# Kernel tuning notes

Measured on AMD Instinct MI355X. Metric: run time of the kernel, lower is better.

Reference implementation:

```python
import jax, jax.numpy as jnp
import numpy as np
import math

B, N, K, S = 4, 128, 250, 250   # batch, channels(d_model), chunk len, num chunks
M = 64 // 2                      # d_state complex modes (conjugate-pair S4D param.)


def setup_inputs() -> dict:
    key = jax.random.key(0)
    ks = jax.random.split(key, 24)
    d = {"x": jax.random.normal(ks[0], (B, N, K, S), jnp.float32)}
    i = 1
    for p in ("intra", "inter"):
        # S4D (diagonal SSM) parameters
        d[p + "_log_dt"] = (jax.random.uniform(ks[i], (N,), jnp.float32)
                            * (math.log(0.1) - math.log(0.001)) + math.log(0.001))
        d[p + "_logA_re"] = jnp.full((N, M), math.log(0.5), jnp.float32)
        d[p + "_A_im"] = jnp.tile(math.pi * jnp.arange(M, dtype=jnp.float32), (N, 1))
        d[p + "_C_re"] = jax.random.normal(ks[i + 1], (N, M), jnp.float32) * (0.5 ** 0.5)
        d[p + "_C_im"] = jax.random.normal(ks[i + 2], (N, M), jnp.float32) * (0.5 ** 0.5)
        d[p + "_D"] = jax.random.normal(ks[i + 3], (N,), jnp.float32)
        # S4 output position-wise linear (H -> 2H) + GLU
        d[p + "_ow"] = jax.random.normal(ks[i + 4], (2 * N, N), jnp.float32) / math.sqrt(N)
        d[p + "_ob"] = jnp.zeros((2 * N,), jnp.float32)
        # block linear
        d[p + "_lw"] = jax.random.normal(ks[i + 5], (N, N), jnp.float32) / math.sqrt(N)
        d[p + "_lb"] = jnp.zeros((N,), jnp.float32)
        # GroupNorm(1, N)
        d[p + "_gg"] = jnp.ones((N,), jnp.float32)
        d[p + "_gb"] = jnp.zeros((N,), jnp.float32)
        i += 6
    return d


def _s4(u, log_dt, logA_re, A_im, C_re, C_im, D, ow, ob):
    # u: [b, H, L] (transposed layout). S4D kernel + FFT conv + GELU + GLU out.
    L = u.shape[-1]
    dt = jnp.exp(log_dt)                              # [H]
    A = -jnp.exp(logA_re) + 1j * A_im                 # [H, M]
    dtA = dt[:, None] * A                             # [H, M]
    C = (C_re + 1j * C_im) * (jnp.exp(dtA) - 1.0) / A # ZOH-discretized C
    vand = jnp.exp(dtA[:, :, None] * jnp.arange(L, dtype=jnp.float32))  # [H, M, L]
    kern = 2.0 * jnp.einsum('hm,hml->hl', C, vand).real                 # [H, L]
    n = 2 * L
    y = jnp.fft.irfft(jnp.fft.rfft(u, n) * jnp.fft.rfft(kern, n), n)[..., :L]
    y = y + D[:, None] * u
    y = jax.nn.gelu(y)
    y = jnp.einsum('oh,bhl->bol', ow, y) + ob[None, :, None]            # [b, 2H, L]
    y1, y2 = jnp.split(y, 2, axis=1)
    return y1 * jax.nn.sigmoid(y2)                                      # GLU -> [b, H, L]


def _group_norm(x, g, b, eps=1e-8):
    mu = jnp.mean(x, axis=(1, 2, 3), keepdims=True)
    var = jnp.var(x, axis=(1, 2, 3), keepdims=True)
    return (x - mu) / jnp.sqrt(var + eps) * g[None, :, None, None] + b[None, :, None, None]


def reference(x,
              intra_log_dt, intra_logA_re, intra_A_im, intra_C_re, intra_C_im,
              intra_D, intra_ow, intra_ob, intra_lw, intra_lb, intra_gg, intra_gb,
              inter_log_dt, inter_logA_re, inter_A_im, inter_C_re, inter_C_im,
              inter_D, inter_ow, inter_ob, inter_lw, inter_lb, inter_gg, inter_gb):
    Bx, Nx, Kx, Sx = x.shape
    # intra (within-chunk) path: sequence length = K
    intra = jnp.transpose(x, (0, 3, 1, 2)).reshape(Bx * Sx, Nx, Kx)
    intra = _s4(intra, intra_log_dt, intra_logA_re, intra_A_im,
                intra_C_re, intra_C_im, intra_D, intra_ow, intra_ob)
    # faithful to torch: .view(B*S*K, -1) on contiguous [B*S, N, K]
    intra = (intra.reshape(Bx * Sx * Kx, -1) @ intra_lw.T + intra_lb).reshape(Bx * Sx, Nx, Kx)
    intra = jnp.transpose(intra.reshape(Bx, Sx, Nx, Kx), (0, 2, 3, 1))  # [B,N,K,S]
    intra = _group_norm(intra, intra_gg, intra_gb) + x
    # inter (across-chunk) path: sequence length = S
    inter = jnp.transpose(intra, (0, 2, 1, 3)).reshape(Bx * Kx, Nx, Sx)
    inter = _s4(inter, inter_log_dt, inter_logA_re, inter_A_im,
                inter_C_re, inter_C_im, inter_D, inter_ow, inter_ob)
    inter = (inter.reshape(Bx * Kx * Sx, -1) @ inter_lw.T + inter_lb).reshape(Bx * Kx, Nx, Sx)
    inter = jnp.transpose(inter.reshape(Bx, Kx, Nx, Sx), (0, 2, 1, 3))  # [B,N,K,S]
    inter = _group_norm(inter, inter_gg, inter_gb)
    return inter + intra
```

## Files before the change

kernel.cpp:

```cpp
#include <hip/hip_runtime.h>
#include <math.h>

#define NTOT 32000000

typedef __attribute__((ext_vector_type(8))) short bf8_t;
typedef __attribute__((ext_vector_type(4))) float f4_t;

__device__ __forceinline__ float fast_tanh(float t) {
    return 1.0f - 2.0f / (1.0f + __expf(2.0f * t));
}
__device__ __forceinline__ float gelu_f(float v) {
    return 0.5f * v * (1.0f + fast_tanh(0.7978845608028654f * (v + 0.044715f * v * v * v)));
}
__device__ __forceinline__ float sigmoid_f(float v) {
    return 1.0f / (1.0f + __expf(-v));
}
__device__ __forceinline__ unsigned short f2bf(float f) {
    unsigned u = __float_as_uint(f);
    u = (u + 0x7FFFu + ((u >> 16) & 1u)) >> 16;
    return (unsigned short)u;
}
__device__ __forceinline__ float bf2f(unsigned short u) {
    return __uint_as_float(((unsigned)u) << 16);
}
__device__ __forceinline__ unsigned swz(unsigned a) {
    return a ^ (((a >> 9) & 7u) << 4);
}

__global__ void wc_kernel(const float* __restrict__ log_dt, const float* __restrict__ logA_re,
                          const float* __restrict__ A_im, const float* __restrict__ C_re,
                          const float* __restrict__ C_im, float* __restrict__ wC) {
    int t = blockIdx.x * 256 + threadIdx.x;
    if (t >= 128 * 32) return;
    int h = t >> 5, m = t & 31;
    float dt  = expf(log_dt[h]);
    float are = -expf(logA_re[t]);
    float aim = A_im[t];
    float er  = expf(dt * are);
    float wr  = er * cosf(dt * aim);
    float wi  = er * sinf(dt * aim);
    float e1r = wr - 1.0f, e1i = wi;
    float inv = 1.0f / (are * are + aim * aim);
    float qr  = (e1r * are + e1i * aim) * inv;
    float qi  = (e1i * are - e1r * aim) * inv;
    float cre = C_re[t], cim = C_im[t];
    wC[h * 128 + m]      = dt * are;
    wC[h * 128 + 32 + m] = dt * aim;
    wC[h * 128 + 64 + m] = 2.0f * (cre * qr - cim * qi);
    wC[h * 128 + 96 + m] = 2.0f * (cre * qi + cim * qr);
}

__global__ void kern_kernel(const float* __restrict__ wC, const float* __restrict__ Dv,
                            float* __restrict__ kern) {
    int h = blockIdx.x, l = threadIdx.x;
    const float* wc = wC + (h << 7);
    float acc = 0.0f;
    if (l < 250) {
        float fl = (float)l;
#pragma unroll 1
        for (int m = 0; m < 32; ++m) {
            float er  = expf(wc[m] * fl);
            float ang = wc[32 + m] * fl;
            float sv, cv;
            sincosf(ang, &sv, &cv);
            acc += er * (wc[64 + m] * cv - wc[96 + m] * sv);
        }
        if (l == 0) acc += Dv[h];
    }
    kern[(h << 8) + l] = acc;
}

__global__ void frag_kernel(const float* __restrict__ kern, unsigned short* __restrict__ fragH,
                            unsigned short* __restrict__ fragL) {
    int h = blockIdx.x, d16 = blockIdx.y, lane = threadIdx.x;
    int lid = lane & 15, q = lane >> 4;
    const float* kh = kern + (h << 8);
    bf8_t vh, vl;
#pragma unroll
    for (int j = 0; j < 8; ++j) {
        int idx = d16 * 16 + lid - 8 * q - j;
        float v = (idx >= 0) ? kh[idx] : 0.0f;
        unsigned short hb = f2bf(v);
        vh[j] = (short)hb;
        vl[j] = (short)f2bf(v - bf2f(hb));
    }
    long off = ((long)((h << 4) + d16) * 64 + lane) * 8;
    *(bf8_t*)(fragH + off) = vh;
    *(bf8_t*)(fragL + off) = vl;
}

__global__ void cvtw_kernel(const float* __restrict__ ow, const float* __restrict__ lw,
                            unsigned short* __restrict__ owbf, unsigned short* __restrict__ lwbf) {
    int t = blockIdx.x * 256 + threadIdx.x;
    if (t < 32768) owbf[t] = f2bf(ow[t]);
    else if (t < 49152) lwbf[t - 32768] = f2bf(lw[t - 32768]);
}

__global__ __launch_bounds__(256, 3)
void conv_kernel(const float* __restrict__ in, unsigned short* __restrict__ Y,
                 const unsigned short* __restrict__ fragH, const unsigned short* __restrict__ fragL,
                 int inter) {
    __shared__ unsigned short Bhi[64 * 256];
    __shared__ unsigned short Blo[64 * 40];
    const int tid = threadIdx.x;
    const int lane = tid & 63, wave = tid >> 6;
    const int lid = lane & 15, quad = lane >> 4;
    const int a = wave >> 1, p = wave & 1;
    const int s0 = blockIdx.x * 64;
    const int h = blockIdx.y, b = blockIdx.z;
    const float* src = in + (long)(b * 128 + h) * 62500;
    char* BhiB = (char*)Bhi;
    char* BloB = (char*)Blo;

    f4_t acc[4][4];
#pragma unroll
    for (int rt = 0; rt < 4; ++rt)
#pragma unroll
        for (int ct = 0; ct < 4; ++ct) acc[rt][ct] = (f4_t)0.0f;

    float2 pf[4];
    auto loadc = [&](int c) {
        if (!inter) {
#pragma unroll
            for (int it = 0; it < 4; ++it) {
                int i = tid + it * 256;
                int kk = i >> 5;
                int sp = (i & 31) << 1;
                int k = (c << 5) + kk;
                bool v = (k < 250) && (s0 + sp < 250);
                pf[it] = v ? *(const float2*)(src + (long)k * 250 + s0 + sp)
                           : make_float2(0.0f, 0.0f);
            }
        } else {
#pragma unroll
            for (int it = 0; it < 4; ++it) {
                int i = tid + it * 256;
                int sq = i >> 4;
                int tt = (i & 15) << 1;
                int t = (c << 5) + tt;
                bool v = (s0 + sq < 250) && (t < 250);
                pf[it] = v ? *(const float2*)(src + (long)(s0 + sq) * 250 + t)
                           : make_float2(0.0f, 0.0f);
            }
        }
    };
    auto storec = [&](int c) {
        if (!inter) {
#pragma unroll
            for (int it = 0; it < 4; ++it) {
                int i = tid + it * 256;
                int kk = i >> 5;
                int sp = (i & 31) << 1;
                int k = (c << 5) + kk;
                unsigned short hx = f2bf(pf[it].x);
                unsigned short hy = f2bf(pf[it].y);
                unsigned b0 = (unsigned)(sp * 512 + k * 2) ^ ((unsigned)(sp & 7) << 4);
                unsigned b1 = (unsigned)((sp + 1) * 512 + k * 2) ^ ((unsigned)((sp + 1) & 7) << 4);
                *(unsigned short*)(BhiB + b0) = hx;
                *(unsigned short*)(BhiB + b1) = hy;
                Blo[sp * 40 + kk] = f2bf(pf[it].x - bf2f(hx));
                Blo[(sp + 1) * 40 + kk] = f2bf(pf[it].y - bf2f(hy));
            }
        } else {
#pragma unroll
            for (int it = 0; it < 4; ++it) {
                int i = tid + it * 256;
                int sq = i >> 4;
                int tt = (i & 15) << 1;
                unsigned short hx = f2bf(pf[it].x);
                unsigned short hy = f2bf(pf[it].y);
                unsigned hpack = (unsigned)hx | ((unsigned)hy << 16);
                unsigned b0 = (unsigned)(sq * 512 + ((c << 5) + tt) * 2) ^ ((unsigned)(sq & 7) << 4);
                *(unsigned*)(BhiB + b0) = hpack;
                unsigned short lx = f2bf(pf[it].x - bf2f(hx));
                unsigned short ly = f2bf(pf[it].y - bf2f(hy));
                *(unsigned*)(BloB + sq * 80 + tt * 2) = (unsigned)lx | ((unsigned)ly << 16);
            }
        }
    };

    loadc(0);
#pragma unroll 1
    for (int c = 0; c < 8; ++c) {
        __syncthreads();
        storec(c);
        __syncthreads();
        if (c < 7) loadc(c + 1);
        bf8_t bh[4], bl[4];
#pragma unroll
        for (int ct = 0; ct < 4; ++ct) {
            int row = ct * 16 + lid;
            unsigned byteB = (unsigned)(row * 512 + c * 64 + quad * 16) ^ ((unsigned)(row & 7) << 4);
            bh[ct] = *(const bf8_t*)(BhiB + byteB);
            bl[ct] = *(const bf8_t*)(BloB + row * 80 + quad * 16);
        }
#pragma unroll
        for (int rt = 0; rt < 4; ++rt) {
            int n = 2 * rt + a - c;
            if (n >= 0) {
                long fo = ((long)((h << 4) + 2 * n + p) * 64 + lane) * 8;
                bf8_t fh = *(const bf8_t*)(fragH + fo);
                bf8_t fl = *(const bf8_t*)(fragL + fo);
#pragma unroll
                for (int ct = 0; ct < 4; ++ct) {
                    acc[rt][ct] = __builtin_amdgcn_mfma_f32_16x16x32_bf16(fh, bh[ct], acc[rt][ct], 0, 0, 0);
                    acc[rt][ct] = __builtin_amdgcn_mfma_f32_16x16x32_bf16(fh, bl[ct], acc[rt][ct], 0, 0, 0);
                    acc[rt][ct] = __builtin_amdgcn_mfma_f32_16x16x32_bf16(fl, bh[ct], acc[rt][ct], 0, 0, 0);
                }
            }
        }
    }
    __syncthreads();
#pragma unroll
    for (int rt = 0; rt < 4; ++rt) {
        const int l0 = rt * 64 + wave * 16 + quad * 4;
#pragma unroll
        for (int ct = 0; ct < 4; ++ct) {
            const int sq = ct * 16 + lid;
            unsigned lo = (unsigned)f2bf(gelu_f(acc[rt][ct][0])) |
                          ((unsigned)f2bf(gelu_f(acc[rt][ct][1])) << 16);
            unsigned hi = (unsigned)f2bf(gelu_f(acc[rt][ct][2])) |
                          ((unsigned)f2bf(gelu_f(acc[rt][ct][3])) << 16);
            unsigned byteO = (unsigned)(sq * 512 + l0 * 2) ^ ((unsigned)(sq & 7) << 4);
            *(uint2*)(BhiB + byteO) = make_uint2(lo, hi);
        }
    }
    __syncthreads();
    unsigned int* Yg = (unsigned int*)Y + ((long)(b * 250 + s0) * 128 + h) * 125;
#pragma unroll 1
    for (int i = tid; i < 8192; i += 256) {
        int sq = i >> 7, e = i & 127;
        if (e < 125 && s0 + sq < 250) {
            unsigned v = *(unsigned*)(BhiB + ((unsigned)(sq * 512 + e * 4) ^ ((unsigned)(sq & 7) << 4)));
            Yg[(long)sq * 16000 + e] = v;
        }
    }
}

__global__ __launch_bounds__(256, 2)
void mlp_kernel(const unsigned short* __restrict__ Ybf, const unsigned short* __restrict__ owbf,
                const float* __restrict__ ob, const unsigned short* __restrict__ lwbf,
                const float* __restrict__ lb, float* __restrict__ V, double* __restrict__ part) {
    __shared__ unsigned short ZL[32768];
    __shared__ unsigned short Yt[32 * 136];
    const int tid = threadIdx.x;
    const int lane = tid & 63, wave = tid >> 6;
    const int lid = lane & 15, quad = lane >> 4;
    const int seq = blockIdx.x;
    const unsigned short* Ys = Ybf + (long)seq * 32000;

    const int tb0 = 2 * wave;
    int tmap[4] = {tb0, tb0 + 1, tb0 + 8, tb0 + 9};
    bf8_t wf[4][4];
#pragma unroll
    for (int c = 0; c < 4; ++c)
#pragma unroll
        for (int t = 0; t < 4; ++t)
            wf[c][t] = *(const bf8_t*)(owbf + (tmap[t] * 16 + lid) * 128 + c * 32 + quad * 8);
    float ob1[2][4], ob2[2][4];
#pragma unroll
    for (int pp = 0; pp < 2; ++pp)
#pragma unroll
        for (int reg = 0; reg < 4; ++reg) {
            int o = tmap[pp] * 16 + quad * 4 + reg;
            ob1[pp][reg] = ob[o];
            ob2[pp][reg] = ob[128 + o];
        }

    unsigned int pf[8];
    auto loadc = [&](int l0) {
#pragma unroll
        for (int it = 0; it < 8; ++it) {
            int i = tid + it * 256;
            int hh = i >> 4;
            int l = l0 + (i & 15) * 2;
            pf[it] = (l < 250) ? *(const unsigned int*)(Ys + hh * 250 + l) : 0u;
        }
    };
    auto storec = [&]() {
#pragma unroll
        for (int it = 0; it < 8; ++it) {
            int i = tid + it * 256;
            int hh = i >> 4;
            int l2 = (i & 15) * 2;
            Yt[l2 * 136 + hh] = (unsigned short)(pf[it] & 0xFFFF);
            Yt[(l2 + 1) * 136 + hh] = (unsigned short)(pf[it] >> 16);
        }
    };

    loadc(0);
#pragma unroll 1
    for (int ch = 0; ch < 8; ++ch) {
        __syncthreads();
        storec();
        __syncthreads();
        if (ch < 7) loadc((ch + 1) * 32);
        f4_t acc[4][2];
#pragma unroll
        for (int t = 0; t < 4; ++t)
#pragma unroll
            for (int jj = 0; jj < 2; ++jj) acc[t][jj] = (f4_t)0.0f;
#pragma unroll
        for (int c = 0; c < 4; ++c) {
            bf8_t bfr[2];
#pragma unroll
            for (int jj = 0; jj < 2; ++jj)
                bfr[jj] = *(const bf8_t*)(Yt + (jj * 16 + lid) * 136 + c * 32 + quad * 8);
#pragma unroll
            for (int t = 0; t < 4; ++t)
#pragma unroll
                for (int jj = 0; jj < 2; ++jj)
                    acc[t][jj] = __builtin_amdgcn_mfma_f32_16x16x32_bf16(wf[c][t], bfr[jj], acc[t][jj], 0, 0, 0);
        }
        const int lbase = ch * 32;
#pragma unroll
        for (int pp = 0; pp < 2; ++pp) {
#pragma unroll
            for (int reg = 0; reg < 4; ++reg) {
                int o = tmap[pp] * 16 + quad * 4 + reg;
#pragma unroll
                for (int jj = 0; jj < 2; ++jj) {
                    int l = lbase + jj * 16 + lid;
                    if (l < 250) {
                        float z1 = acc[pp][jj][reg] + ob1[pp][reg];
                        float z2 = acc[pp + 2][jj][reg] + ob2[pp][reg];
                        unsigned aB = swz((unsigned)(o * 250 + l) * 2u);
                        *(unsigned short*)((char*)ZL + aB) = f2bf(z1 * sigmoid_f(z2));
                    }
                }
            }
        }
    }
    __syncthreads();

    f4_t acc2[4][8];
#pragma unroll
    for (int mt = 0; mt < 4; ++mt)
#pragma unroll
        for (int nt = 0; nt < 8; ++nt) acc2[mt][nt] = (f4_t)0.0f;
    const int j0 = wave * 64;
#pragma unroll
    for (int c = 0; c < 4; ++c) {
        bf8_t af[4];
#pragma unroll
        for (int mt = 0; mt < 4; ++mt) {
            unsigned aB = swz((unsigned)((j0 + mt * 16 + lid) * 128 + c * 32 + quad * 8) * 2u);
            af[mt] = *(const bf8_t*)((char*)ZL + aB);
        }
#pragma unroll
        for (int nt = 0; nt < 8; ++nt) {
            bf8_t bfr = *(const bf8_t*)(lwbf + (nt * 16 + lid) * 128 + c * 32 + quad * 8);
#pragma unroll
            for (int mt = 0; mt < 4; ++mt)
                acc2[mt][nt] = __builtin_amdgcn_mfma_f32_16x16x32_bf16(af[mt], bfr, acc2[mt][nt], 0, 0, 0);
        }
    }
    double s = 0.0, q = 0.0;
    float* Vs = V + (long)seq * 32000;
#pragma unroll
    for (int nt = 0; nt < 8; ++nt) {
        int o = nt * 16 + lid;
        float bb = lb[o];
#pragma unroll
        for (int mt = 0; mt < 4; ++mt)
#pragma unroll
            for (int reg = 0; reg < 4; ++reg) {
                int j = j0 + mt * 16 + quad * 4 + reg;
                if (j < 250) {
                    float v = acc2[mt][nt][reg] + bb;
                    Vs[j * 128 + o] = v;
                    s += (double)v;
                    q += (double)v * (double)v;
                }
            }
    }
    __syncthreads();
    double* red = (double*)Yt;
    red[tid] = s;
    red[256 + tid] = q;
    __syncthreads();
    for (int st = 128; st > 0; st >>= 1) {
        if (tid < st) {
            red[tid] += red[tid + st];
            red[256 + tid] += red[256 + tid + st];
        }
        __syncthreads();
    }
    if (tid == 0) {
        part[seq * 2] = red[0];
        part[seq * 2 + 1] = red[256];
    }
}

__global__ void stats_final_kernel(const double* __restrict__ part, float* __restrict__ stats) {
    __shared__ double ssum[256], ssq[256];
    const int b = blockIdx.x;
    double s = 0.0, q = 0.0;
    if (threadIdx.x < 250) {
        s = part[(b * 250 + threadIdx.x) * 2];
        q = part[(b * 250 + threadIdx.x) * 2 + 1];
    }
    ssum[threadIdx.x] = s; ssq[threadIdx.x] = q;
    __syncthreads();
    for (int st = 128; st > 0; st >>= 1) {
        if (threadIdx.x < st) {
            ssum[threadIdx.x] += ssum[threadIdx.x + st];
            ssq[threadIdx.x]  += ssq[threadIdx.x + st];
        }
        __syncthreads();
    }
    if (threadIdx.x == 0) {
        double mu = ssum[0] / 8000000.0;
        double var = ssq[0] / 8000000.0 - mu * mu;
        stats[b * 2] = (float)mu;
        stats[b * 2 + 1] = (float)(1.0 / sqrt(var + 1e-8));
    }
}

__global__ void intra_fin_kernel(const float* __restrict__ f, const float* __restrict__ x,
                                 const float* __restrict__ stats, const float* __restrict__ gg,
                                 const float* __restrict__ gb, float* __restrict__ out) {
    __shared__ float tile[32][33];
    int kt = blockIdx.x, st = blockIdx.y;
    int bn = blockIdx.z; int b = bn >> 7, n = bn & 127;
    int tx = threadIdx.x & 31, ty = threadIdx.x >> 5;
    const float mu = stats[b * 2], rs = stats[b * 2 + 1];
    const float ga = gg[n] * rs, bb = gb[n];
    const float* fb = f + (long)(b * 250) * 32000 + n * 250;
#pragma unroll
    for (int j = 0; j < 4; ++j) {
        int k = kt * 32 + tx;
        int s = st * 32 + ty + j * 8;
        if (k < 250 && s < 250) tile[ty + j * 8][tx] = fb[(long)s * 32000 + k];
    }
    __syncthreads();
#pragma unroll
    for (int j = 0; j < 4; ++j) {
        int s = st * 32 + tx;
        int k = kt * 32 + ty + j * 8;
        if (k < 250 && s < 250) {
            long idx = ((long)(b * 128 + n) * 250 + k) * 250 + s;
            out[idx] = (tile[tx][ty + j * 8] - mu) * ga + bb + x[idx];
        }
    }
}

__global__ void final_kernel(const float* __restrict__ f2, const float* __restrict__ stats,
                             const float* __restrict__ gg, const float* __restrict__ gb,
                             float* __restrict__ out) {
    long g = (long)blockIdx.x * 256 + threadIdx.x;
    if (g >= NTOT) return;
    int s = (int)(g % 250); long r = g / 250;
    int k = (int)(r % 250); long bn = r / 250;
    int n = (int)(bn % 128); int b = (int)(bn / 128);
    float mu = stats[b * 2], rs = stats[b * 2 + 1];
    float v = f2[((long)(b * 250 + k) * 128 + n) * 250 + s];
    out[g] = (v - mu) * rs * gg[n] + gb[n] + out[g];
}

extern "C" void kernel_launch(void* const* d_in, const int* in_sizes, int n_in,
                              void* d_out, int out_size, void* d_ws, size_t ws_size,
                              hipStream_t stream) {
    (void)in_sizes; (void)n_in; (void)out_size; (void)ws_size;
    const float* x = (const float*)d_in[0];
    float* out = (float*)d_out;
    char* base = (char*)d_ws;
    float* V            = (float*)base;
    unsigned short* Ybf = (unsigned short*)(base + 128000000L);
    float* wC           = (float*)(base + 256000000L);
    unsigned short* owbf= (unsigned short*)(base + 256065536L);
    unsigned short* lwbf= (unsigned short*)(base + 256131072L);
    double* part        = (double*)(base + 256163840L);
    float* stats        = (float*)(base + 256180224L);
    float* kern         = (float*)(base + 118000000L);
    unsigned short* fragH = (unsigned short*)(base + 120000000L);
    unsigned short* fragL = (unsigned short*)(base + 123000000L);

    const float* i_logdt = (const float*)d_in[1];
    const float* i_logA  = (const float*)d_in[2];
    const float* i_Aim   = (const float*)d_in[3];
    const float* i_Cre   = (const float*)d_in[4];
    const float* i_Cim   = (const float*)d_in[5];
    const float* i_D     = (const float*)d_in[6];
    const float* i_ow    = (const float*)d_in[7];
    const float* i_ob    = (const float*)d_in[8];
    const float* i_lw    = (const float*)d_in[9];
    const float* i_lb    = (const float*)d_in[10];
    const float* i_gg    = (const float*)d_in[11];
    const float* i_gb    = (const float*)d_in[12];
    const float* e_logdt = (const float*)d_in[13];
    const float* e_logA  = (const float*)d_in[14];
    const float* e_Aim   = (const float*)d_in[15];
    const float* e_Cre   = (const float*)d_in[16];
    const float* e_Cim   = (const float*)d_in[17];
    const float* e_D     = (const float*)d_in[18];
    const float* e_ow    = (const float*)d_in[19];
    const float* e_ob    = (const float*)d_in[20];
    const float* e_lw    = (const float*)d_in[21];
    const float* e_lb    = (const float*)d_in[22];
    const float* e_gg    = (const float*)d_in[23];
    const float* e_gb    = (const float*)d_in[24];

    wc_kernel<<<16, 256, 0, stream>>>(i_logdt, i_logA, i_Aim, i_Cre, i_Cim, wC);
    kern_kernel<<<128, 256, 0, stream>>>(wC, i_D, kern);
    frag_kernel<<<dim3(128, 16), 64, 0, stream>>>(kern, fragH, fragL);
    cvtw_kernel<<<192, 256, 0, stream>>>(i_ow, i_lw, owbf, lwbf);
    conv_kernel<<<dim3(4, 128, 4), 256, 0, stream>>>(x, Ybf, fragH, fragL, 0);
    mlp_kernel<<<1000, 256, 0, stream>>>(Ybf, owbf, i_ob, lwbf, i_lb, V, part);
    stats_final_kernel<<<4, 256, 0, stream>>>(part, stats);
    intra_fin_kernel<<<dim3(8, 8, 512), 256, 0, stream>>>(V, x, stats, i_gg, i_gb, out);

    wc_kernel<<<16, 256, 0, stream>>>(e_logdt, e_logA, e_Aim, e_Cre, e_Cim, wC);
    kern_kernel<<<128, 256, 0, stream>>>(wC, e_D, kern);
    frag_kernel<<<dim3(128, 16), 64, 0, stream>>>(kern, fragH, fragL);
    cvtw_kernel<<<192, 256, 0, stream>>>(e_ow, e_lw, owbf, lwbf);
    conv_kernel<<<dim3(4, 128, 4), 256, 0, stream>>>(out, Ybf, fragH, fragL, 1);
    mlp_kernel<<<1000, 256, 0, stream>>>(Ybf, owbf, e_ob, lwbf, e_lb, V, part);
    stats_final_kernel<<<4, 256, 0, stream>>>(part, stats);
    final_kernel<<<NTOT / 256, 256, 0, stream>>>(V, stats, e_gg, e_gb, out);
}
```

Measured before the change: 841.1 us.

## Split MLP kernel across two blocks per sequence and repad LDS swizzles

The MLP kernel is split into two blocks per sequence, each handling half of the GLU hidden channels, which halves its LDS footprint so more blocks can be resident (launch bounds raised to 3). Partial statistics move from double to float and the stats reducer now sums 500 partials. The conv kernel's LDS layouts switch from padding to an XOR swizzle, with packed 8-byte stores of four consecutive k values, and its launch bound is raised to 4 blocks. The aim is higher occupancy and fewer LDS bank conflicts, at the cost of float accumulation in the partial sums and possible register spilling under the tighter bounds.

After: 1.085 ms. +29.0%, slower.

```diff
diff --git a/kernel.cpp b/kernel.cpp
--- a/kernel.cpp
+++ b/kernel.cpp
@@ -25,6 +25,9 @@
 }
 __device__ __forceinline__ unsigned swz(unsigned a) {
     return a ^ (((a >> 9) & 7u) << 4);
+}
+__device__ __forceinline__ unsigned fxor(int row) {
+    return ((unsigned)(row & 1) << 6) ^ ((unsigned)((row >> 1) & 7) << 4);
 }
 
 __global__ void wc_kernel(const float* __restrict__ log_dt, const float* __restrict__ logA_re,
@@ -96,12 +99,12 @@
     else if (t < 49152) lwbf[t - 32768] = f2bf(lw[t - 32768]);
 }
 
-__global__ __launch_bounds__(256, 3)
+__global__ __launch_bounds__(256, 4)
 void conv_kernel(const float* __restrict__ in, unsigned short* __restrict__ Y,
                  const unsigned short* __restrict__ fragH, const unsigned short* __restrict__ fragL,
                  int inter) {
     __shared__ unsigned short Bhi[64 * 256];
-    __shared__ unsigned short Blo[64 * 40];
+    __shared__ unsigned short Blo[64 * 64];
     const int tid = threadIdx.x;
     const int lane = tid & 63, wave = tid >> 6;
     const int lid = lane & 15, quad = lane >> 4;
@@ -111,6 +114,8 @@
     const float* src = in + (long)(b * 128 + h) * 62500;
     char* BhiB = (char*)Bhi;
     char* BloB = (char*)Blo;
+    const int q8 = tid >> 5;
+    const int spL = (tid & 31) << 1;
 
     f4_t acc[4][4];
 #pragma unroll
@@ -123,12 +128,9 @@
         if (!inter) {
 #pragma unroll
             for (int it = 0; it < 4; ++it) {
-                int i = tid + it * 256;
-                int kk = i >> 5;
-                int sp = (i & 31) << 1;
-                int k = (c << 5) + kk;
-                bool v = (k < 250) && (s0 + sp < 250);
-                pf[it] = v ? *(const float2*)(src + (long)k * 250 + s0 + sp)
+                int k = (c << 5) + q8 * 4 + it;
+                bool v = (k < 250) && (s0 + spL < 250);
+                pf[it] = v ? *(const float2*)(src + (long)k * 250 + s0 + spL)
                            : make_float2(0.0f, 0.0f);
             }
         } else {
@@ -146,21 +148,30 @@
     };
     auto storec = [&](int c) {
         if (!inter) {
+            unsigned wx0 = 0, wx1 = 0, wy0 = 0, wy1 = 0;
+            unsigned lx0 = 0, lx1 = 0, ly0 = 0, ly1 = 0;
 #pragma unroll
             for (int it = 0; it < 4; ++it) {
-                int i = tid + it * 256;
-                int kk = i >> 5;
-                int sp = (i & 31) << 1;
-                int k = (c << 5) + kk;
-                unsigned short hx = f2bf(pf[it].x);
-                unsigned short hy = f2bf(pf[it].y);
-                unsigned b0 = (unsigned)(sp * 512 + k * 2) ^ ((unsigned)(sp & 7) << 4);
-                unsigned b1 = (unsigned)((sp + 1) * 512 + k * 2) ^ ((unsigned)((sp + 1) & 7) << 4);
-                *(unsigned short*)(BhiB + b0) = hx;
-                *(unsigned short*)(BhiB + b1) = hy;
-                Blo[sp * 40 + kk] = f2bf(pf[it].x - bf2f(hx));
-                Blo[(sp + 1) * 40 + kk] = f2bf(pf[it].y - bf2f(hy));
-            }
+                unsigned short hx = f2bf(pf[it].x), hy = f2bf(pf[it].y);
+                unsigned short lx = f2bf(pf[it].x - bf2f(hx));
+                unsigned short ly = f2bf(pf[it].y - bf2f(hy));
+                if (it < 2) {
+                    wx0 |= (unsigned)hx << (16 * it); wy0 |= (unsigned)hy << (16 * it);
+                    lx0 |= (unsigned)lx << (16 * it); ly0 |= (unsigned)ly << (16 * it);
+                } else {
+                    wx1 |= (unsigned)hx << (16 * (it - 2)); wy1 |= (unsigned)hy << (16 * (it - 2));
+                    lx1 |= (unsigned)lx << (16 * (it - 2)); ly1 |= (unsigned)ly << (16 * (it - 2));
+                }
+            }
+            unsigned colB = (unsigned)((c << 6) + (q8 << 3));
+            unsigned a0 = ((unsigned)(spL * 512) + colB) ^ fxor(spL);
+            unsigned a1 = ((unsigned)((spL + 1) * 512) + colB) ^ fxor(spL + 1);
+            *(uint2*)(BhiB + a0) = make_uint2(wx0, wx1);
+            *(uint2*)(BhiB + a1) = make_uint2(wy0, wy1);
+            unsigned c0 = ((unsigned)(spL * 128) + (unsigned)(q8 << 3)) ^ fxor(spL);
+            unsigned c1 = ((unsigned)((spL + 1) * 128) + (unsigned)(q8 << 3)) ^ fxor(spL + 1);
+            *(uint2*)(BloB + c0) = make_uint2(lx0, lx1);
+            *(uint2*)(BloB + c1) = make_uint2(ly0, ly1);
         } else {
 #pragma unroll
             for (int it = 0; it < 4; ++it) {
@@ -169,12 +180,12 @@
                 int tt = (i & 15) << 1;
                 unsigned short hx = f2bf(pf[it].x);
                 unsigned short hy = f2bf(pf[it].y);
-                unsigned hpack = (unsigned)hx | ((unsigned)hy << 16);
-                unsigned b0 = (unsigned)(sq * 512 + ((c << 5) + tt) * 2) ^ ((unsigned)(sq & 7) << 4);
-                *(unsigned*)(BhiB + b0) = hpack;
+                unsigned b0 = ((unsigned)(sq * 512 + ((c << 5) + tt) * 2)) ^ fxor(sq);
+                *(unsigned*)(BhiB + b0) = (unsigned)hx | ((unsigned)hy << 16);
                 unsigned short lx = f2bf(pf[it].x - bf2f(hx));
                 unsigned short ly = f2bf(pf[it].y - bf2f(hy));
-                *(unsigned*)(BloB + sq * 80 + tt * 2) = (unsigned)lx | ((unsigned)ly << 16);
+                unsigned b1 = ((unsigned)(sq * 128 + tt * 2)) ^ fxor(sq);
+                *(unsigned*)(BloB + b1) = (unsigned)lx | ((unsigned)ly << 16);
             }
         }
     };
@@ -190,9 +201,8 @@
 #pragma unroll
         for (int ct = 0; ct < 4; ++ct) {
             int row = ct * 16 + lid;
-            unsigned byteB = (unsigned)(row * 512 + c * 64 + quad * 16) ^ ((unsigned)(row & 7) << 4);
-            bh[ct] = *(const bf8_t*)(BhiB + byteB);
-            bl[ct] = *(const bf8_t*)(BloB + row * 80 + quad * 16);
+            bh[ct] = *(const bf8_t*)(BhiB + (((unsigned)(row * 512 + c * 64 + quad * 16)) ^ fxor(row)));
+            bl[ct] = *(const bf8_t*)(BloB + (((unsigned)(row * 128 + quad * 16)) ^ fxor(row)));
         }
 #pragma unroll
         for (int rt = 0; rt < 4; ++rt) {
@@ -221,7 +231,7 @@
                           ((unsigned)f2bf(gelu_f(acc[rt][ct][1])) << 16);
             unsigned hi = (unsigned)f2bf(gelu_f(acc[rt][ct][2])) |
                           ((unsigned)f2bf(gelu_f(acc[rt][ct][3])) << 16);
-            unsigned byteO = (unsigned)(sq * 512 + l0 * 2) ^ ((unsigned)(sq & 7) << 4);
+            unsigned byteO = ((unsigned)(sq * 512 + l0 * 2)) ^ fxor(sq);
             *(uint2*)(BhiB + byteO) = make_uint2(lo, hi);
         }
     }
@@ -231,41 +241,41 @@
     for (int i = tid; i < 8192; i += 256) {
         int sq = i >> 7, e = i & 127;
         if (e < 125 && s0 + sq < 250) {
-            unsigned v = *(unsigned*)(BhiB + ((unsigned)(sq * 512 + e * 4) ^ ((unsigned)(sq & 7) << 4)));
+            unsigned v = *(unsigned*)(BhiB + (((unsigned)(sq * 512 + e * 4)) ^ fxor(sq)));
             Yg[(long)sq * 16000 + e] = v;
         }
     }
 }
 
-__global__ __launch_bounds__(256, 2)
+__global__ __launch_bounds__(256, 3)
 void mlp_kernel(const unsigned short* __restrict__ Ybf, const unsigned short* __restrict__ owbf,
                 const float* __restrict__ ob, const unsigned short* __restrict__ lwbf,
-                const float* __restrict__ lb, float* __restrict__ V, double* __restrict__ part) {
-    __shared__ unsigned short ZL[32768];
-    __shared__ unsigned short Yt[32 * 136];
+                const float* __restrict__ lb, float* __restrict__ V, float* __restrict__ part) {
+    __shared__ unsigned short ZL[16000];
+    __shared__ unsigned short Yt[32 * 128];
     const int tid = threadIdx.x;
     const int lane = tid & 63, wave = tid >> 6;
     const int lid = lane & 15, quad = lane >> 4;
-    const int seq = blockIdx.x;
+    const int seq = blockIdx.x, hf = blockIdx.y;
     const unsigned short* Ys = Ybf + (long)seq * 32000;
-
-    const int tb0 = 2 * wave;
-    int tmap[4] = {tb0, tb0 + 1, tb0 + 8, tb0 + 9};
-    bf8_t wf[4][4];
-#pragma unroll
-    for (int c = 0; c < 4; ++c)
-#pragma unroll
-        for (int t = 0; t < 4; ++t)
-            wf[c][t] = *(const bf8_t*)(owbf + (tmap[t] * 16 + lid) * 128 + c * 32 + quad * 8);
-    float ob1[2][4], ob2[2][4];
-#pragma unroll
-    for (int pp = 0; pp < 2; ++pp)
-#pragma unroll
-        for (int reg = 0; reg < 4; ++reg) {
-            int o = tmap[pp] * 16 + quad * 4 + reg;
-            ob1[pp][reg] = ob[o];
-            ob2[pp][reg] = ob[128 + o];
-        }
+    char* YtB = (char*)Yt;
+    char* ZLB = (char*)ZL;
+
+    const int tA = 4 * hf + wave;
+    const int tB = 8 + 4 * hf + wave;
+    bf8_t wf[4][2];
+#pragma unroll
+    for (int c = 0; c < 4; ++c) {
+        wf[c][0] = *(const bf8_t*)(owbf + (tA * 16 + lid) * 128 + c * 32 + quad * 8);
+        wf[c][1] = *(const bf8_t*)(owbf + (tB * 16 + lid) * 128 + c * 32 + quad * 8);
+    }
+    float ob1[4], ob2[4];
+#pragma unroll
+    for (int reg = 0; reg < 4; ++reg) {
+        int hp = wave * 16 + quad * 4 + reg;
+        ob1[reg] = ob[64 * hf + hp];
+        ob2[reg] = ob[128 + 64 * hf + hp];
+    }
 
     unsigned int pf[8];
     auto loadc = [&](int l0) {
@@ -283,8 +293,10 @@
             int i = tid + it * 256;
             int hh = i >> 4;
             int l2 = (i & 15) * 2;
-            Yt[l2 * 136 + hh] = (unsigned short)(pf[it] & 0xFFFF);
-            Yt[(l2 + 1) * 136 + hh] = (unsigned short)(pf[it] >> 16);
+            unsigned a0 = ((unsigned)(l2 * 256 + hh * 2)) ^ fxor(l2);
+            unsigned a1 = ((unsigned)((l2 + 1) * 256 + hh * 2)) ^ fxor(l2 + 1);
+            *(unsigned short*)(YtB + a0) = (unsigned short)(pf[it] & 0xFFFF);
+            *(unsigned short*)(YtB + a1) = (unsigned short)(pf[it] >> 16);
         }
     };
 
@@ -295,87 +307,87 @@
         storec();
         __syncthreads();
         if (ch < 7) loadc((ch + 1) * 32);
-        f4_t acc[4][2];
-#pragma unroll
-        for (int t = 0; t < 4; ++t)
-#pragma unroll
-            for (int jj = 0; jj < 2; ++jj) acc[t][jj] = (f4_t)0.0f;
+        f4_t acc[2][2];
+#pragma unroll
+        for (int pp = 0; pp < 2; ++pp)
+#pragma unroll
+            for (int jj = 0; jj < 2; ++jj) acc[pp][jj] = (f4_t)0.0f;
 #pragma unroll
         for (int c = 0; c < 4; ++c) {
             bf8_t bfr[2];
 #pragma unroll
-            for (int jj = 0; jj < 2; ++jj)
-                bfr[jj] = *(const bf8_t*)(Yt + (jj * 16 + lid) * 136 + c * 32 + quad * 8);
-#pragma unroll
-            for (int t = 0; t < 4; ++t)
+            for (int jj = 0; jj < 2; ++jj) {
+                int row = jj * 16 + lid;
+                bfr[jj] = *(const bf8_t*)(YtB + (((unsigned)(row * 256 + c * 64 + quad * 16)) ^ fxor(row)));
+            }
+#pragma unroll
+            for (int pp = 0; pp < 2; ++pp)
 #pragma unroll
                 for (int jj = 0; jj < 2; ++jj)
-                    acc[t][jj] = __builtin_amdgcn_mfma_f32_16x16x32_bf16(wf[c][t], bfr[jj], acc[t][jj], 0, 0, 0);
+                    acc[pp][jj] = __builtin_amdgcn_mfma_f32_16x16x32_bf16(wf[c][pp], bfr[jj], acc[pp][jj], 0, 0, 0);
         }
         const int lbase = ch * 32;
 #pragma unroll
-        for (int pp = 0; pp < 2; ++pp) {
-#pragma unroll
-            for (int reg = 0; reg < 4; ++reg) {
-                int o = tmap[pp] * 16 + quad * 4 + reg;
-#pragma unroll
-                for (int jj = 0; jj < 2; ++jj) {
-                    int l = lbase + jj * 16 + lid;
-                    if (l < 250) {
-                        float z1 = acc[pp][jj][reg] + ob1[pp][reg];
-                        float z2 = acc[pp + 2][jj][reg] + ob2[pp][reg];
-                        unsigned aB = swz((unsigned)(o * 250 + l) * 2u);
-                        *(unsigned short*)((char*)ZL + aB) = f2bf(z1 * sigmoid_f(z2));
-                    }
+        for (int reg = 0; reg < 4; ++reg) {
+            int hp = wave * 16 + quad * 4 + reg;
+#pragma unroll
+            for (int jj = 0; jj < 2; ++jj) {
+                int l = lbase + jj * 16 + lid;
+                if (l < 250) {
+                    float z1 = acc[0][jj][reg] + ob1[reg];
+                    float z2 = acc[1][jj][reg] + ob2[reg];
+                    unsigned aB = swz((unsigned)(hp * 250 + l) * 2u);
+                    *(unsigned short*)(ZLB + aB) = f2bf(z1 * sigmoid_f(z2));
                 }
             }
         }
     }
     __syncthreads();
 
-    f4_t acc2[4][8];
-#pragma unroll
-    for (int mt = 0; mt < 4; ++mt)
+    f4_t acc2[2][8];
+#pragma unroll
+    for (int mt = 0; mt < 2; ++mt)
 #pragma unroll
         for (int nt = 0; nt < 8; ++nt) acc2[mt][nt] = (f4_t)0.0f;
-    const int j0 = wave * 64;
+    const int jl0 = wave * 32;
 #pragma unroll
     for (int c = 0; c < 4; ++c) {
-        bf8_t af[4];
-#pragma unroll
-        for (int mt = 0; mt < 4; ++mt) {
-            unsigned aB = swz((unsigned)((j0 + mt * 16 + lid) * 128 + c * 32 + quad * 8) * 2u);
-            af[mt] = *(const bf8_t*)((char*)ZL + aB);
+        bf8_t af[2];
+#pragma unroll
+        for (int mt = 0; mt < 2; ++mt) {
+            int jl = jl0 + mt * 16 + lid;
+            if (jl > 124) jl = 124;
+            af[mt] = *(const bf8_t*)(ZLB + swz((unsigned)(jl * 128 + c * 32 + quad * 8) * 2u));
         }
 #pragma unroll
         for (int nt = 0; nt < 8; ++nt) {
             bf8_t bfr = *(const bf8_t*)(lwbf + (nt * 16 + lid) * 128 + c * 32 + quad * 8);
 #pragma unroll
-            for (int mt = 0; mt < 4; ++mt)
+            for (int mt = 0; mt < 2; ++mt)
                 acc2[mt][nt] = __builtin_amdgcn_mfma_f32_16x16x32_bf16(af[mt], bfr, acc2[mt][nt], 0, 0, 0);
         }
     }
-    double s = 0.0, q = 0.0;
-    float* Vs = V + (long)seq * 32000;
+    float s = 0.0f, q = 0.0f;
+    float* Vs = V + (long)seq * 32000 + hf * 16000;
 #pragma unroll
     for (int nt = 0; nt < 8; ++nt) {
         int o = nt * 16 + lid;
         float bb = lb[o];
 #pragma unroll
-        for (int mt = 0; mt < 4; ++mt)
+        for (int mt = 0; mt < 2; ++mt)
 #pragma unroll
             for (int reg = 0; reg < 4; ++reg) {
-                int j = j0 + mt * 16 + quad * 4 + reg;
-                if (j < 250) {
+                int jlr = jl0 + mt * 16 + quad * 4 + reg;
+                if (jlr < 125) {
                     float v = acc2[mt][nt][reg] + bb;
-                    Vs[j * 128 + o] = v;
-                    s += (double)v;
-                    q += (double)v * (double)v;
+                    Vs[jlr * 128 + o] = v;
+                    s += v;
+                    q += v * v;
                 }
             }
     }
     __syncthreads();
-    double* red = (double*)Yt;
+    float* red = (float*)Yt;
     red[tid] = s;
     red[256 + tid] = q;
     __syncthreads();
@@ -387,18 +399,18 @@
         __syncthreads();
     }
     if (tid == 0) {
-        part[seq * 2] = red[0];
-        part[seq * 2 + 1] = red[256];
-    }
-}
-
-__global__ void stats_final_kernel(const double* __restrict__ part, float* __restrict__ stats) {
+        part[(seq * 2 + hf) * 2]     = red[0];
+        part[(seq * 2 + hf) * 2 + 1] = red[256];
+    }
+}
+
+__global__ void stats_final_kernel(const float* __restrict__ part, float* __restrict__ stats) {
     __shared__ double ssum[256], ssq[256];
     const int b = blockIdx.x;
     double s = 0.0, q = 0.0;
-    if (threadIdx.x < 250) {
-        s = part[(b * 250 + threadIdx.x) * 2];
-        q = part[(b * 250 + threadIdx.x) * 2 + 1];
+    for (int i = threadIdx.x; i < 500; i += 256) {
+        s += (double)part[(b * 500 + i) * 2];
+        q += (double)part[(b * 500 + i) * 2 + 1];
     }
     ssum[threadIdx.x] = s; ssq[threadIdx.x] = q;
     __syncthreads();
@@ -470,7 +482,7 @@
     float* wC           = (float*)(base + 256000000L);
     unsigned short* owbf= (unsigned short*)(base + 256065536L);
     unsigned short* lwbf= (unsigned short*)(base + 256131072L);
-    double* part        = (double*)(base + 256163840L);
+    float* part         = (float*)(base + 256163840L);
     float* stats        = (float*)(base + 256180224L);
     float* kern         = (float*)(base + 118000000L);
     unsigned short* fragH = (unsigned short*)(base + 120000000L);
@@ -506,7 +518,7 @@
     frag_kernel<<<dim3(128, 16), 64, 0, stream>>>(kern, fragH, fragL);
     cvtw_kernel<<<192, 256, 0, stream>>>(i_ow, i_lw, owbf, lwbf);
     conv_kernel<<<dim3(4, 128, 4), 256, 0, stream>>>(x, Ybf, fragH, fragL, 0);
-    mlp_kernel<<<1000, 256, 0, stream>>>(Ybf, owbf, i_ob, lwbf, i_lb, V, part);
+    mlp_kernel<<<dim3(1000, 2), 256, 0, stream>>>(Ybf, owbf, i_ob, lwbf, i_lb, V, part);
     stats_final_kernel<<<4, 256, 0, stream>>>(part, stats);
     intra_fin_kernel<<<dim3(8, 8, 512), 256, 0, stream>>>(V, x, stats, i_gg, i_gb, out);
 
@@ -515,7 +527,7 @@
     frag_kernel<<<dim3(128, 16), 64, 0, stream>>>(kern, fragH, fragL);
     cvtw_kernel<<<192, 256, 0, stream>>>(e_ow, e_lw, owbf, lwbf);
     conv_kernel<<<dim3(4, 128, 4), 256, 0, stream>>>(out, Ybf, fragH, fragL, 1);
-    mlp_kernel<<<1000, 256, 0, stream>>>(Ybf, owbf, e_ob, lwbf, e_lb, V, part);
+    mlp_kernel<<<dim3(1000, 2), 256, 0, stream>>>(Ybf, owbf, e_ob, lwbf, e_lb, V, part);
     stats_final_kernel<<<4, 256, 0, stream>>>(part, stats);
     final_kernel<<<NTOT / 256, 256, 0, stream>>>(V, stats, e_gg, e_gb, out);
 }
```
